# Optimization experiments

Measured on AMD Instinct MI355X. Metric: run time of the kernel, lower is better.

The kernel has to match this reference:

```python
import jax, jax.numpy as jnp
import numpy as np

B, N, C, H = 8, 1024, 1024, 16
D = C // H
DFF = 4 * C
EPS = 1e-6


def _ln(x):
    mu = jnp.mean(x, axis=-1, keepdims=True)
    var = jnp.mean(jnp.square(x - mu), axis=-1, keepdims=True)
    return (x - mu) / jnp.sqrt(var + EPS)


def _modulate(x, shift, scale):
    return x * (1 + scale) + shift


def setup_inputs() -> dict:
    key = jax.random.key(0)
    ks = jax.random.split(key, 12)
    s = 0.02
    inp = {
        "x": jax.random.normal(ks[0], (B, N, C), jnp.float32),
        "c": jax.random.normal(ks[1], (B, 1, C), jnp.float32),
        "causal_mask": jnp.tril(jnp.ones((N, N), jnp.int32))[None, None],  # [1,1,N,N]
        "qkv_w": jax.random.normal(ks[2], (3 * C, C), jnp.float32) * s,
        "qkv_b": jnp.zeros((3 * C,), jnp.float32),
        "proj_w": jax.random.normal(ks[3], (C, C), jnp.float32) * s,
        "proj_b": jnp.zeros((C,), jnp.float32),
        "fc1_w": jax.random.normal(ks[4], (DFF, C), jnp.float32) * s,
        "fc1_b": jnp.zeros((DFF,), jnp.float32),
        "fc2_w": jax.random.normal(ks[5], (C, DFF), jnp.float32) * s,
        "fc2_b": jnp.zeros((C,), jnp.float32),
        "ada_w": jax.random.normal(ks[6], (6 * C, C), jnp.float32) * s,
        "ada_b": jnp.zeros((6 * C,), jnp.float32),
    }
    return inp


def reference(x, c, causal_mask, qkv_w, qkv_b, proj_w, proj_b,
              fc1_w, fc1_b, fc2_w, fc2_b, ada_w, ada_b):
    # adaLN modulation: SiLU -> Linear(C -> 6C) -> chunk 6
    mod = jax.nn.silu(c) @ ada_w.T + ada_b  # [B,1,6C]
    (shift_msa, scale_msa, gate_msa,
     shift_mlp, scale_mlp, gate_mlp) = jnp.split(mod, 6, axis=-1)

    # --- causal attention ---
    y = _modulate(_ln(x), shift_msa, scale_msa)  # [B,N,C]
    qkv = y @ qkv_w.T + qkv_b                    # [B,N,3C]
    qkv = qkv.reshape(B, N, 3, H, D).transpose(2, 0, 3, 1, 4)  # [3,B,H,N,D]
    q, k, v = qkv[0], qkv[1], qkv[2]
    scale = D ** -0.5
    attn = jnp.einsum('bhnd,bhmd->bhnm', q, k) * scale  # [B,H,N,N]
    attn = jnp.where(causal_mask == 0, -jnp.inf, attn)
    attn = jax.nn.softmax(attn, axis=-1)
    o = jnp.einsum('bhnm,bhmd->bhnd', attn, v)
    o = o.transpose(0, 2, 1, 3).reshape(B, N, C)
    o = o @ proj_w.T + proj_b
    x = x + gate_msa * o

    # --- MLP ---
    z = _modulate(_ln(x), shift_mlp, scale_mlp)
    h = jax.nn.gelu(z @ fc1_w.T + fc1_b, approximate=True)
    m = h @ fc2_w.T + fc2_b
    x = x + gate_mlp * m
    return x
```

## Files before the change

kernel.cpp:

```cpp
#include <hip/hip_runtime.h>
#include <math.h>
#include <stdint.h>
#include <stddef.h>

namespace {

constexpr int kB = 8, kN = 1024, kC = 1024, kH = 16, kD = 64, kDFF = 4096;
constexpr int kM = kB * kN;
constexpr int k6C = 6 * kC;
constexpr float kQKScale = 0.18033688011112042f;
constexpr float kM8 = 8.0f;

typedef _Float16 half8 __attribute__((ext_vector_type(8)));
typedef _Float16 half4v __attribute__((ext_vector_type(4)));
typedef float f32x4 __attribute__((ext_vector_type(4)));
typedef int v4i __attribute__((ext_vector_type(4)));
typedef signed char i8;

__device__ inline void ld_lds16(const void* g, void* l) {
  __builtin_amdgcn_global_load_lds(
      (const __attribute__((address_space(1))) void*)g,
      (__attribute__((address_space(3))) void*)l, 16, 0, 0);
}

__device__ inline int xcd_swizzle(int flat, int nwg) {
  return (flat & 7) * (nwg >> 3) + (flat >> 3);
}

__device__ inline unsigned pack4_i8(float y0, float y1, float y2, float y3, float inv) {
  int q0 = (int)rintf(y0 * inv), q1 = (int)rintf(y1 * inv);
  int q2 = (int)rintf(y2 * inv), q3 = (int)rintf(y3 * inv);
  q0 = min(max(q0, -127), 127); q1 = min(max(q1, -127), 127);
  q2 = min(max(q2, -127), 127); q3 = min(max(q3, -127), 127);
  return (unsigned)(q0 & 0xFF) | ((unsigned)(q1 & 0xFF) << 8) |
         ((unsigned)(q2 & 0xFF) << 16) | ((unsigned)(q3 & 0xFF) << 24);
}

__global__ void cvt_f32_f16(const float* __restrict__ src, _Float16* __restrict__ dst) {
  size_t i = (size_t)blockIdx.x * 256 + threadIdx.x;
  float4 f = ((const float4*)src)[i];
  half4v h;
  h[0] = (_Float16)f.x; h[1] = (_Float16)f.y; h[2] = (_Float16)f.z; h[3] = (_Float16)f.w;
  ((half4v*)dst)[i] = h;
}

__global__ __launch_bounds__(256) void quant_w_kernel(
    const float* __restrict__ src, i8* __restrict__ dst, float* __restrict__ wscale) {
  int n = blockIdx.x, tid = threadIdx.x;
  const float* row = src + (size_t)n * kC;
  float4 f = ((const float4*)row)[tid];
  float m = fmaxf(fmaxf(fabsf(f.x), fabsf(f.y)), fmaxf(fabsf(f.z), fabsf(f.w)));
#pragma unroll
  for (int msk = 32; msk; msk >>= 1) m = fmaxf(m, __shfl_xor(m, msk));
  __shared__ float red[4];
  int w = tid >> 6, lane = tid & 63;
  if (lane == 0) red[w] = m;
  __syncthreads();
  m = fmaxf(fmaxf(red[0], red[1]), fmaxf(red[2], red[3]));
  m = fmaxf(m, 1e-12f);
  float inv = 127.f / m;
  ((unsigned*)(dst + (size_t)n * kC))[tid] = pack4_i8(f.x, f.y, f.z, f.w, inv);
  if (tid == 0) wscale[n] = m * (1.f / 127.f);
}

__global__ __launch_bounds__(256) void mod_kernel(
    const float* __restrict__ c, const float* __restrict__ ada_w,
    const float* __restrict__ ada_b, float* __restrict__ mod) {
  __shared__ float sc[kC];
  int b  = blockIdx.x / (k6C / 4);
  int j0 = (blockIdx.x % (k6C / 4)) * 4;
  int tid = threadIdx.x;
  for (int i = tid; i < kC; i += 256) {
    float v = c[b * kC + i];
    sc[i] = v / (1.f + expf(-v));
  }
  __syncthreads();
  int w = tid >> 6, lane = tid & 63;
  int j = j0 + w;
  const float* wr = ada_w + (size_t)j * kC;
  float acc = 0.f;
#pragma unroll
  for (int kk = 0; kk < kC / 64; ++kk) {
    int k = kk * 64 + lane;
    acc += sc[k] * wr[k];
  }
#pragma unroll
  for (int m = 32; m; m >>= 1) acc += __shfl_xor(acc, m);
  if (lane == 0) mod[b * k6C + j] = acc + ada_b[j];
}

template <typename T>
__global__ __launch_bounds__(256) void ln_mod_q_kernel(
    const T* __restrict__ x, const float* __restrict__ mod,
    i8* __restrict__ out, float* __restrict__ ascale,
    int shift_off, int scale_off) {
  int row = blockIdx.x;
  int b = row >> 10;
  const T* xr = x + (size_t)row * kC;
  int tid = threadIdx.x;
  int cc0 = tid * 4;
  float v[4];
  float s = 0.f, s2 = 0.f;
#pragma unroll
  for (int i = 0; i < 4; ++i) {
    v[i] = (float)xr[cc0 + i];
    s += v[i];
    s2 += v[i] * v[i];
  }
#pragma unroll
  for (int m = 32; m; m >>= 1) { s += __shfl_xor(s, m); s2 += __shfl_xor(s2, m); }
  __shared__ float red[8];
  __shared__ float redm[4];
  int w = tid >> 6, lane = tid & 63;
  if (lane == 0) { red[w] = s; red[4 + w] = s2; }
  __syncthreads();
  s  = red[0] + red[1] + red[2] + red[3];
  s2 = red[4] + red[5] + red[6] + red[7];
  float mu   = s * (1.f / kC);
  float var  = s2 * (1.f / kC) - mu * mu;
  float rstd = rsqrtf(var + 1e-6f);
  const float* mb = mod + (size_t)b * k6C;
  float y[4];
  float m = 0.f;
#pragma unroll
  for (int i = 0; i < 4; ++i) {
    y[i] = (v[i] - mu) * rstd * (1.f + mb[scale_off + cc0 + i]) + mb[shift_off + cc0 + i];
    m = fmaxf(m, fabsf(y[i]));
  }
#pragma unroll
  for (int msk = 32; msk; msk >>= 1) m = fmaxf(m, __shfl_xor(m, msk));
  if (lane == 0) redm[w] = m;
  __syncthreads();
  m = fmaxf(fmaxf(redm[0], redm[1]), fmaxf(redm[2], redm[3]));
  m = fmaxf(m, 1e-12f);
  float inv = 127.f / m;
  ((unsigned*)(out + (size_t)row * kC))[tid] = pack4_i8(y[0], y[1], y[2], y[3], inv);
  if (tid == 0) ascale[row] = m * (1.f / 127.f);
}

template <int EPI>
__global__ __launch_bounds__(256, 4) void gemm_i8_kernel(
    const i8* __restrict__ A, const i8* __restrict__ W,
    const float* __restrict__ ascale, const float* __restrict__ wscale,
    const float* __restrict__ bias, _Float16* __restrict__ outp,
    int M, int Nn, int K) {
  __shared__ __align__(16) i8 S[2 * 2 * 128 * 64];
  int tid = threadIdx.x;
  int nwg = (int)(gridDim.x * gridDim.y);
  int swz = xcd_swizzle((int)(blockIdx.y * gridDim.x + blockIdx.x), nwg);
  int bn = swz % (int)gridDim.x, bm = swz / (int)gridDim.x;
  int lane = tid & 63, w = tid >> 6;
  int l15 = lane & 15, quad = lane >> 4;
  int wr = (w >> 1) * 64, wc = (w & 1) * 64;

  v4i acc[4][4];
#pragma unroll
  for (int i = 0; i < 4; ++i)
#pragma unroll
    for (int j = 0; j < 4; ++j) acc[i][j] = (v4i){0, 0, 0, 0};

  const i8* Ag = A + (size_t)bm * 128 * K;
  const i8* Wg = W + (size_t)bn * 128 * K;
  int rg = lane >> 2;
  int gsl = lane & 3;

  int nk = K >> 6;
  {
    i8* As0 = S;
    i8* Bs0 = S + 128 * 64;
#pragma unroll
    for (int s = 0; s < 2; ++s) {
      int row = w * 32 + s * 16 + rg;
      int gc = (gsl ^ ((row >> 1) & 3)) * 16;
      ld_lds16(&Ag[(size_t)row * K + gc], &As0[(w * 32 + s * 16) * 64]);
      ld_lds16(&Wg[(size_t)row * K + gc], &Bs0[(w * 32 + s * 16) * 64]);
    }
  }
  __syncthreads();

  int cread = (quad ^ ((l15 >> 1) & 3)) * 16;
  for (int t = 0; t < nk; ++t) {
    const i8* As = S + (t & 1) * (2 * 128 * 64);
    const i8* Bs = As + 128 * 64;
    if (t + 1 < nk) {
      i8* Asn = S + ((t + 1) & 1) * (2 * 128 * 64);
      i8* Bsn = Asn + 128 * 64;
      int kt = (t + 1) << 6;
#pragma unroll
      for (int s = 0; s < 2; ++s) {
        int row = w * 32 + s * 16 + rg;
        int gc = (gsl ^ ((row >> 1) & 3)) * 16;
        ld_lds16(&Ag[(size_t)row * K + kt + gc], &Asn[(w * 32 + s * 16) * 64]);
        ld_lds16(&Wg[(size_t)row * K + kt + gc], &Bsn[(w * 32 + s * 16) * 64]);
      }
    }
    v4i af[4], bf[4];
#pragma unroll
    for (int i = 0; i < 4; ++i)
      af[i] = *(const v4i*)&As[(wr + i * 16 + l15) * 64 + cread];
#pragma unroll
    for (int j = 0; j < 4; ++j)
      bf[j] = *(const v4i*)&Bs[(wc + j * 16 + l15) * 64 + cread];
#pragma unroll
    for (int i = 0; i < 4; ++i)
#pragma unroll
      for (int j = 0; j < 4; ++j)
        acc[i][j] = __builtin_amdgcn_mfma_i32_16x16x64_i8(af[i], bf[j], acc[i][j], 0, 0, 0);
    __syncthreads();
  }

  _Float16* Cs = (_Float16*)S;
  int row0 = wr + quad * 4;
  int col0 = wc + l15;
#pragma unroll
  for (int i = 0; i < 4; ++i) {
#pragma unroll
    for (int j = 0; j < 4; ++j) {
      int colL = col0 + j * 16;
      int n = bn * 128 + colL;
      float ws = wscale[n];
      float bv = bias[n];
#pragma unroll
      for (int r = 0; r < 4; ++r) {
        int rowL = row0 + i * 16 + r;
        float as = ascale[bm * 128 + rowL];
        float v = (float)acc[i][j][r] * (as * ws) + bv;
        if constexpr (EPI == 0) {
          if (n < kC) v *= kQKScale;
        } else {
          float u = v + 0.044715f * v * v * v;
          float t = exp2f(-2.302208f * u);
          v = v * __builtin_amdgcn_rcpf(1.f + t);
        }
        Cs[rowL * 128 + (((colL >> 3) ^ (rowL & 7)) << 3) + (colL & 7)] = (_Float16)v;
      }
    }
  }
  __syncthreads();
#pragma unroll
  for (int p = 0; p < 8; ++p) {
    int r = (tid >> 4) + p * 16;
    int cc = tid & 15;
    half8 hv = *(const half8*)&Cs[r * 128 + ((cc ^ (r & 7)) << 3)];
    size_t gm = (size_t)(bm * 128 + r);
    int coff = bn * 128 + cc * 8;
    *(half8*)&outp[gm * Nn + coff] = hv;
  }
}

template <int EPI>
__global__ __launch_bounds__(256) void gemm_f16_kernel(
    const _Float16* __restrict__ A, const _Float16* __restrict__ W,
    const float* __restrict__ bias, void* __restrict__ outp,
    const void* __restrict__ resid, const float* __restrict__ mod,
    int M, int Nn, int K, int gate_off) {
  __shared__ __align__(16) _Float16 S[2 * 2 * 128 * 64];
  int tid = threadIdx.x;
  int nwg = (int)(gridDim.x * gridDim.y);
  int swz = xcd_swizzle((int)(blockIdx.y * gridDim.x + blockIdx.x), nwg);
  int bn = swz % (int)gridDim.x, bm = swz / (int)gridDim.x;
  int lane = tid & 63, w = tid >> 6;
  int l15 = lane & 15, quad = lane >> 4;
  int wr = (w >> 1) * 64, wc = (w & 1) * 64;

  f32x4 acc[4][4];
#pragma unroll
  for (int i = 0; i < 4; ++i)
#pragma unroll
    for (int j = 0; j < 4; ++j) acc[i][j] = (f32x4){0.f, 0.f, 0.f, 0.f};

  const _Float16* Ag = A + (size_t)bm * 128 * K;
  const _Float16* Wg = W + (size_t)bn * 128 * K;
  int r8 = lane >> 3;
  int jc = ((lane & 7) ^ r8) * 8;

  auto stage = [&](int buf, int kt) {
    _Float16* Asn = S + buf * (2 * 128 * 64);
    _Float16* Bsn = Asn + 128 * 64;
#pragma unroll
    for (int u = 0; u < 4; ++u) {
      int row = w * 32 + u * 8 + r8;
      ld_lds16(&Ag[(size_t)row * K + kt + jc], &Asn[(w * 32 + u * 8) * 64]);
      ld_lds16(&Wg[(size_t)row * K + kt + jc], &Bsn[(w * 32 + u * 8) * 64]);
    }
  };

  int nk = K / 64;
  stage(0, 0);
  stage(1, 64);

  for (int t = 0; t < nk; ++t) {
    if (t + 1 < nk) {
      asm volatile("s_waitcnt vmcnt(8)" ::: "memory");
    } else {
      asm volatile("s_waitcnt vmcnt(0)" ::: "memory");
    }
    __builtin_amdgcn_s_barrier();
    __builtin_amdgcn_sched_barrier(0);
    const _Float16* As = S + (t & 1) * (2 * 128 * 64);
    const _Float16* Bs = As + 128 * 64;
    half8 af[2][4], bf[2][4];
#pragma unroll
    for (int kk = 0; kk < 2; ++kk) {
#pragma unroll
      for (int i = 0; i < 4; ++i)
        af[kk][i] = *(const half8*)&As[(wr + i * 16 + l15) * 64 +
                                       (((kk * 4 + quad) ^ (l15 & 7)) * 8)];
#pragma unroll
      for (int j = 0; j < 4; ++j)
        bf[kk][j] = *(const half8*)&Bs[(wc + j * 16 + l15) * 64 +
                                       (((kk * 4 + quad) ^ (l15 & 7)) * 8)];
    }
    asm volatile("s_waitcnt lgkmcnt(0)" ::: "memory");
    __builtin_amdgcn_sched_barrier(0);
    __builtin_amdgcn_s_barrier();
    __builtin_amdgcn_sched_barrier(0);
    if (t + 2 < nk) stage(t & 1, (t + 2) * 64);
#pragma unroll
    for (int kk = 0; kk < 2; ++kk)
#pragma unroll
      for (int i = 0; i < 4; ++i)
#pragma unroll
        for (int j = 0; j < 4; ++j)
          acc[i][j] = __builtin_amdgcn_mfma_f32_16x16x32_f16(af[kk][i], bf[kk][j],
                                                             acc[i][j], 0, 0, 0);
  }

  _Float16* Cs = S;
  int row0 = wr + quad * 4;
  int col0 = wc + l15;
#pragma unroll
  for (int i = 0; i < 4; ++i) {
#pragma unroll
    for (int j = 0; j < 4; ++j) {
      int colL = col0 + j * 16;
      int n = bn * 128 + colL;
      float bv = bias[n];
#pragma unroll
      for (int r = 0; r < 4; ++r) {
        int rowL = row0 + i * 16 + r;
        float v = acc[i][j][r] + bv;
        Cs[rowL * 128 + (((colL >> 3) ^ (rowL & 7)) << 3) + (colL & 7)] = (_Float16)v;
      }
    }
  }
  __syncthreads();
  int b6 = (bm >> 3) * k6C + gate_off + bn * 128;
#pragma unroll
  for (int p = 0; p < 8; ++p) {
    int r = (tid >> 4) + p * 16;
    int cc = tid & 15;
    half8 hv = *(const half8*)&Cs[r * 128 + ((cc ^ (r & 7)) << 3)];
    size_t gm = (size_t)(bm * 128 + r);
    int coff = bn * 128 + cc * 8;
    if constexpr (EPI == 2) {
      const float* rp = &((const float*)resid)[gm * kC + coff];
      const float* gp = &mod[b6 + cc * 8];
      half8 ov;
#pragma unroll
      for (int e = 0; e < 8; ++e) ov[e] = (_Float16)(rp[e] + gp[e] * (float)hv[e]);
      *(half8*)&((_Float16*)outp)[gm * kC + coff] = ov;
    } else {
      const _Float16* rp = &((const _Float16*)resid)[gm * kC + coff];
      const float* gp = &mod[b6 + cc * 8];
      half8 rv = *(const half8*)rp;
      float ov[8];
#pragma unroll
      for (int e = 0; e < 8; ++e) ov[e] = (float)rv[e] + gp[e] * (float)hv[e];
      *(float4*)&((float*)outp)[gm * kC + coff] = *(float4*)&ov[0];
      *(float4*)&((float*)outp)[gm * kC + coff + 4] = *(float4*)&ov[4];
    }
  }
}

__global__ __launch_bounds__(256) void vtrans_kernel(
    const _Float16* __restrict__ qkv, _Float16* __restrict__ vT) {
  int nt = blockIdx.x, h = blockIdx.y, b = blockIdx.z;
  __shared__ _Float16 Ts[64 * 72];
  int tid = threadIdx.x;
  const _Float16* src = qkv + ((size_t)(b * kN + nt * 64)) * (3 * kC) + 2 * kC + h * 64;
#pragma unroll
  for (int u = 0; u < 2; ++u) {
    int idx = tid + u * 256;
    int r = idx >> 3, c8 = (idx & 7) * 8;
    *(uint4*)&Ts[r * 72 + c8] = *(const uint4*)&src[(size_t)r * (3 * kC) + c8];
  }
  __syncthreads();
  _Float16* dst = vT + (((size_t)(b * kH + h)) * 64) * kN + nt * 64;
#pragma unroll
  for (int u = 0; u < 2; ++u) {
    int idx = tid + u * 256;
    int d = idx >> 3, n8 = (idx & 7) * 8;
    half8 v;
#pragma unroll
    for (int e = 0; e < 8; ++e) v[e] = Ts[(n8 + e) * 72 + d];
    *(half8*)&dst[(size_t)d * kN + n8] = v;
  }
}

__global__ __launch_bounds__(256) void attn_kernel(
    const _Float16* __restrict__ qkv, const _Float16* __restrict__ vT,
    _Float16* __restrict__ o) {
  int nwg = (int)(gridDim.x * gridDim.y * gridDim.z);
  int flat = (int)((blockIdx.z * gridDim.y + blockIdx.y) * gridDim.x + blockIdx.x);
  int swz = xcd_swizzle(flat, nwg);
  int qt = swz % (int)gridDim.x;
  int tmp = swz / (int)gridDim.x;
  int h = tmp % (int)gridDim.y, b = tmp / (int)gridDim.y;
  __shared__ __align__(16) _Float16 Qs[128 * 64];
  __shared__ __align__(16) _Float16 Ks[64 * 64];
  __shared__ __align__(16) _Float16 Vs[64 * 64];
  __shared__ __align__(16) _Float16 Ps[128 * 72];
  int tid = threadIdx.x, lane = tid & 63, w = tid >> 6;
  int l15 = lane & 15, quad = lane >> 4;
  int wq = w * 32;
  int r8 = lane >> 3;
  int jc = ((lane & 7) ^ r8) * 8;

  const _Float16* Qg = qkv + ((size_t)(b * kN + qt * 128)) * (3 * kC) + h * kD;
  const _Float16* Kg = qkv + ((size_t)(b * kN)) * (3 * kC) + kC + h * kD;
  const _Float16* Vg = vT + ((size_t)(b * kH + h) * kD) * kN;

#pragma unroll
  for (int u = 0; u < 4; ++u)
    ld_lds16(&Qg[(size_t)(w * 32 + u * 8 + r8) * (3 * kC) + jc],
             &Qs[(w * 32 + u * 8) * 64]);
  __syncthreads();

  half8 aq[2][2];
#pragma unroll
  for (int i = 0; i < 2; ++i)
#pragma unroll
    for (int kk = 0; kk < 2; ++kk)
      aq[i][kk] = *(const half8*)&Qs[(wq + i * 16 + l15) * 64 +
                                     (((kk * 4 + quad) ^ (l15 & 7)) * 8)];

  f32x4 o_acc[2][4];
  f32x4 lsum[2];
#pragma unroll
  for (int i = 0; i < 2; ++i) {
    lsum[i] = (f32x4){0.f, 0.f, 0.f, 0.f};
#pragma unroll
    for (int dt = 0; dt < 4; ++dt) o_acc[i][dt] = (f32x4){0.f, 0.f, 0.f, 0.f};
  }
  half8 ones;
#pragma unroll
  for (int e = 0; e < 8; ++e) ones[e] = (_Float16)1.f;

  int jmax = 2 * qt + 2;
  for (int j = 0; j < jmax; ++j) {
#pragma unroll
    for (int u = 0; u < 2; ++u) {
      int row = w * 16 + u * 8 + r8;
      ld_lds16(&Kg[(size_t)(j * 64 + row) * (3 * kC) + jc], &Ks[(w * 16 + u * 8) * 64]);
      ld_lds16(&Vg[(size_t)row * kN + j * 64 + jc],         &Vs[(w * 16 + u * 8) * 64]);
    }
    __syncthreads();
    bool need_mask = (j >= 2 * qt);

    f32x4 s[2][4];
#pragma unroll
    for (int ct = 0; ct < 4; ++ct) {
      half8 b0 = *(const half8*)&Ks[(ct * 16 + l15) * 64 + ((quad ^ (l15 & 7)) * 8)];
      half8 b1 = *(const half8*)&Ks[(ct * 16 + l15) * 64 + (((4 + quad) ^ (l15 & 7)) * 8)];
#pragma unroll
      for (int i = 0; i < 2; ++i) {
        f32x4 t = (f32x4){0.f, 0.f, 0.f, 0.f};
        t = __builtin_amdgcn_mfma_f32_16x16x32_f16(aq[i][0], b0, t, 0, 0, 0);
        t = __builtin_amdgcn_mfma_f32_16x16x32_f16(aq[i][1], b1, t, 0, 0, 0);
        s[i][ct] = t;
      }
    }

#pragma unroll
    for (int i = 0; i < 2; ++i)
#pragma unroll
      for (int ct = 0; ct < 4; ++ct)
#pragma unroll
        for (int r = 0; r < 4; ++r) {
          float p = exp2f(fminf(s[i][ct][r] - kM8, 14.f));
          if (need_mask) {
            int kg = j * 64 + ct * 16 + l15;
            int qg = qt * 128 + wq + i * 16 + quad * 4 + r;
            if (kg > qg) p = 0.f;
          }
          Ps[(wq + i * 16 + quad * 4 + r) * 72 + ct * 16 + l15] = (_Float16)p;
        }

    half8 ap[2][2];
#pragma unroll
    for (int i = 0; i < 2; ++i) {
      ap[i][0] = *(const half8*)&Ps[(wq + i * 16 + l15) * 72 + quad * 8];
      ap[i][1] = *(const half8*)&Ps[(wq + i * 16 + l15) * 72 + 32 + quad * 8];
      lsum[i] = __builtin_amdgcn_mfma_f32_16x16x32_f16(ap[i][0], ones, lsum[i], 0, 0, 0);
      lsum[i] = __builtin_amdgcn_mfma_f32_16x16x32_f16(ap[i][1], ones, lsum[i], 0, 0, 0);
    }
#pragma unroll
    for (int dt = 0; dt < 4; ++dt) {
      half8 bv0 = *(const half8*)&Vs[(dt * 16 + l15) * 64 + ((quad ^ (l15 & 7)) * 8)];
      half8 bv1 = *(const half8*)&Vs[(dt * 16 + l15) * 64 + (((4 + quad) ^ (l15 & 7)) * 8)];
#pragma unroll
      for (int i = 0; i < 2; ++i) {
        o_acc[i][dt] = __builtin_amdgcn_mfma_f32_16x16x32_f16(ap[i][0], bv0, o_acc[i][dt], 0, 0, 0);
        o_acc[i][dt] = __builtin_amdgcn_mfma_f32_16x16x32_f16(ap[i][1], bv1, o_acc[i][dt], 0, 0, 0);
      }
    }
    __syncthreads();
  }

#pragma unroll
  for (int i = 0; i < 2; ++i) {
    float rl[4];
#pragma unroll
    for (int r = 0; r < 4; ++r) rl[r] = __builtin_amdgcn_rcpf(lsum[i][r]);
#pragma unroll
    for (int dt = 0; dt < 4; ++dt)
#pragma unroll
      for (int r = 0; r < 4; ++r) {
        int q = qt * 128 + wq + i * 16 + quad * 4 + r;
        o[((size_t)(b * kN + q)) * kC + h * kD + dt * 16 + l15] =
            (_Float16)(o_acc[i][dt][r] * rl[r]);
      }
  }
}

}

extern "C" void kernel_launch(void* const* d_in, const int* in_sizes, int n_in,
                              void* d_out, int out_size, void* d_ws, size_t ws_size,
                              hipStream_t stream) {
  const float* x      = (const float*)d_in[0];
  const float* c      = (const float*)d_in[1];
  const float* qkv_w  = (const float*)d_in[3];
  const float* qkv_b  = (const float*)d_in[4];
  const float* proj_w = (const float*)d_in[5];
  const float* proj_b = (const float*)d_in[6];
  const float* fc1_w  = (const float*)d_in[7];
  const float* fc1_b  = (const float*)d_in[8];
  const float* fc2_w  = (const float*)d_in[9];
  const float* fc2_b  = (const float*)d_in[10];
  const float* ada_w  = (const float*)d_in[11];
  const float* ada_b  = (const float*)d_in[12];
  float* out = (float*)d_out;

  char* ws = (char*)d_ws;
  float*    mod     = (float*)(ws);
  i8*       w_qkv   = (i8*)(ws + 196608);
  i8*       w_fc1   = (i8*)(ws + 3342336);
  _Float16* w_proj  = (_Float16*)(ws + 7536640);
  _Float16* w_fc2   = (_Float16*)(ws + 9633792);
  i8*       bufA    = (i8*)(ws + 18022400);
  float*    ascale  = (float*)(ws + 26411008);
  float*    ws_qkv  = (float*)(ws + 26443776);
  float*    ws_fc1  = (float*)(ws + 26456064);
  _Float16* vT      = (_Float16*)(ws + 26509312);
  _Float16* x2h     = (_Float16*)(ws + 26509312);
  _Float16* bufO    = (_Float16*)(ws + 43286528);
  _Float16* qkvh    = (_Float16*)(ws + 60063744);
  _Float16* hbuf    = (_Float16*)(ws + 60063744);

  quant_w_kernel<<<3 * kC, 256, 0, stream>>>(qkv_w, w_qkv, ws_qkv);
  quant_w_kernel<<<kDFF, 256, 0, stream>>>(fc1_w, w_fc1, ws_fc1);
  cvt_f32_f16<<<kC * kC / 1024, 256, 0, stream>>>(proj_w, w_proj);
  cvt_f32_f16<<<kC * kDFF / 1024, 256, 0, stream>>>(fc2_w, w_fc2);
  mod_kernel<<<kB * (k6C / 4), 256, 0, stream>>>(c, ada_w, ada_b, mod);
  ln_mod_q_kernel<float><<<kM, 256, 0, stream>>>(x, mod, bufA, ascale, 0, kC);
  gemm_i8_kernel<0><<<dim3(3 * kC / 128, kM / 128), 256, 0, stream>>>(
      bufA, w_qkv, ascale, ws_qkv, qkv_b, qkvh, kM, 3 * kC, kC);
  vtrans_kernel<<<dim3(kN / 64, kH, kB), 256, 0, stream>>>(qkvh, vT);
  attn_kernel<<<dim3(kN / 128, kH, kB), 256, 0, stream>>>(qkvh, vT, bufO);
  gemm_f16_kernel<2><<<dim3(kC / 128, kM / 128), 256, 0, stream>>>(
      bufO, w_proj, proj_b, x2h, x, mod, kM, kC, kC, 2 * kC);
  ln_mod_q_kernel<_Float16><<<kM, 256, 0, stream>>>(x2h, mod, bufA, ascale, 3 * kC, 4 * kC);
  gemm_i8_kernel<1><<<dim3(kDFF / 128, kM / 128), 256, 0, stream>>>(
      bufA, w_fc1, ascale, ws_fc1, fc1_b, hbuf, kM, kDFF, kC);
  gemm_f16_kernel<3><<<dim3(kC / 128, kM / 128), 256, 0, stream>>>(
      hbuf, w_fc2, fc2_b, out, x2h, mod, kM, kC, kDFF, 5 * kC);
}
```

Measured before the change: 467.3 us.

## Deepen prefetch pipelines in int8 GEMM and attention with vmcnt-based waits

The int8 GEMM main loop now issues its global-to-LDS loads two K-tiles ahead instead of one. It waits with explicit vmcnt counters and uses a single barrier per step, placed after the fragment reads, before reissuing loads into the freed buffer. The attention kernel double-buffers its K/V tiles in one merged shared array and prefetches tile j+2 once the current V fragments are in registers. It also raises launch bounds to three blocks per CU. The aim is to hide global load latency behind MFMA work, at the cost of hand-tuned waitcnt logic that could race if the counts are wrong, plus more LDS and register pressure.

```diff
diff --git a/kernel.cpp b/kernel.cpp
--- a/kernel.cpp
+++ b/kernel.cpp
@@ -164,36 +164,33 @@
   int rg = lane >> 2;
   int gsl = lane & 3;
 
-  int nk = K >> 6;
-  {
-    i8* As0 = S;
-    i8* Bs0 = S + 128 * 64;
+  auto stage = [&](int buf, int kt) {
+    i8* As = S + buf * (2 * 128 * 64);
+    i8* Bs = As + 128 * 64;
 #pragma unroll
     for (int s = 0; s < 2; ++s) {
       int row = w * 32 + s * 16 + rg;
       int gc = (gsl ^ ((row >> 1) & 3)) * 16;
-      ld_lds16(&Ag[(size_t)row * K + gc], &As0[(w * 32 + s * 16) * 64]);
-      ld_lds16(&Wg[(size_t)row * K + gc], &Bs0[(w * 32 + s * 16) * 64]);
-    }
-  }
-  __syncthreads();
+      ld_lds16(&Ag[(size_t)row * K + kt + gc], &As[(w * 32 + s * 16) * 64]);
+      ld_lds16(&Wg[(size_t)row * K + kt + gc], &Bs[(w * 32 + s * 16) * 64]);
+    }
+  };
+
+  int nk = K >> 6;
+  stage(0, 0);
+  stage(1, 64);
 
   int cread = (quad ^ ((l15 >> 1) & 3)) * 16;
   for (int t = 0; t < nk; ++t) {
+    if (t + 1 < nk) {
+      asm volatile("s_waitcnt vmcnt(4)" ::: "memory");
+    } else {
+      asm volatile("s_waitcnt vmcnt(0)" ::: "memory");
+    }
+    __builtin_amdgcn_s_barrier();
+    __builtin_amdgcn_sched_barrier(0);
     const i8* As = S + (t & 1) * (2 * 128 * 64);
     const i8* Bs = As + 128 * 64;
-    if (t + 1 < nk) {
-      i8* Asn = S + ((t + 1) & 1) * (2 * 128 * 64);
-      i8* Bsn = Asn + 128 * 64;
-      int kt = (t + 1) << 6;
-#pragma unroll
-      for (int s = 0; s < 2; ++s) {
-        int row = w * 32 + s * 16 + rg;
-        int gc = (gsl ^ ((row >> 1) & 3)) * 16;
-        ld_lds16(&Ag[(size_t)row * K + kt + gc], &Asn[(w * 32 + s * 16) * 64]);
-        ld_lds16(&Wg[(size_t)row * K + kt + gc], &Bsn[(w * 32 + s * 16) * 64]);
-      }
-    }
     v4i af[4], bf[4];
 #pragma unroll
     for (int i = 0; i < 4; ++i)
@@ -201,12 +198,16 @@
 #pragma unroll
     for (int j = 0; j < 4; ++j)
       bf[j] = *(const v4i*)&Bs[(wc + j * 16 + l15) * 64 + cread];
+    asm volatile("s_waitcnt lgkmcnt(0)" ::: "memory");
+    __builtin_amdgcn_sched_barrier(0);
+    __builtin_amdgcn_s_barrier();
+    __builtin_amdgcn_sched_barrier(0);
+    if (t + 2 < nk) stage(t & 1, (t + 2) << 6);
 #pragma unroll
     for (int i = 0; i < 4; ++i)
 #pragma unroll
       for (int j = 0; j < 4; ++j)
         acc[i][j] = __builtin_amdgcn_mfma_i32_16x16x64_i8(af[i], bf[j], acc[i][j], 0, 0, 0);
-    __syncthreads();
   }
 
   _Float16* Cs = (_Float16*)S;
@@ -398,7 +399,7 @@
   }
 }
 
-__global__ __launch_bounds__(256) void attn_kernel(
+__global__ __launch_bounds__(256, 3) void attn_kernel(
     const _Float16* __restrict__ qkv, const _Float16* __restrict__ vT,
     _Float16* __restrict__ o) {
   int nwg = (int)(gridDim.x * gridDim.y * gridDim.z);
@@ -407,10 +408,8 @@
   int qt = swz % (int)gridDim.x;
   int tmp = swz / (int)gridDim.x;
   int h = tmp % (int)gridDim.y, b = tmp / (int)gridDim.y;
-  __shared__ __align__(16) _Float16 Qs[128 * 64];
-  __shared__ __align__(16) _Float16 Ks[64 * 64];
-  __shared__ __align__(16) _Float16 Vs[64 * 64];
-  __shared__ __align__(16) _Float16 Ps[128 * 72];
+  __shared__ __align__(16) _Float16 S[2 * 8192 + 128 * 72];
+  _Float16* Ps = S + 16384;
   int tid = threadIdx.x, lane = tid & 63, w = tid >> 6;
   int l15 = lane & 15, quad = lane >> 4;
   int wq = w * 32;
@@ -421,19 +420,34 @@
   const _Float16* Kg = qkv + ((size_t)(b * kN)) * (3 * kC) + kC + h * kD;
   const _Float16* Vg = vT + ((size_t)(b * kH + h) * kD) * kN;
 
+  auto stage_kv = [&](_Float16* dstK, int j) {
+#pragma unroll
+    for (int u = 0; u < 2; ++u) {
+      int row = w * 16 + u * 8 + r8;
+      ld_lds16(&Kg[(size_t)(j * 64 + row) * (3 * kC) + jc], &dstK[(w * 16 + u * 8) * 64]);
+      ld_lds16(&Vg[(size_t)row * kN + j * 64 + jc], &dstK[4096 + (w * 16 + u * 8) * 64]);
+    }
+  };
+
 #pragma unroll
   for (int u = 0; u < 4; ++u)
     ld_lds16(&Qg[(size_t)(w * 32 + u * 8 + r8) * (3 * kC) + jc],
-             &Qs[(w * 32 + u * 8) * 64]);
-  __syncthreads();
+             &S[(w * 32 + u * 8) * 64]);
+  stage_kv(S + 8192, 0);
+  asm volatile("s_waitcnt vmcnt(4)" ::: "memory");
+  __builtin_amdgcn_s_barrier();
 
   half8 aq[2][2];
 #pragma unroll
   for (int i = 0; i < 2; ++i)
 #pragma unroll
     for (int kk = 0; kk < 2; ++kk)
-      aq[i][kk] = *(const half8*)&Qs[(wq + i * 16 + l15) * 64 +
-                                     (((kk * 4 + quad) ^ (l15 & 7)) * 8)];
+      aq[i][kk] = *(const half8*)&S[(wq + i * 16 + l15) * 64 +
+                                    (((kk * 4 + quad) ^ (l15 & 7)) * 8)];
+  asm volatile("s_waitcnt lgkmcnt(0)" ::: "memory");
+  __builtin_amdgcn_sched_barrier(0);
+  __builtin_amdgcn_s_barrier();
+  stage_kv(S, 1);
 
   f32x4 o_acc[2][4];
   f32x4 lsum[2];
@@ -449,13 +463,15 @@
 
   int jmax = 2 * qt + 2;
   for (int j = 0; j < jmax; ++j) {
-#pragma unroll
-    for (int u = 0; u < 2; ++u) {
-      int row = w * 16 + u * 8 + r8;
-      ld_lds16(&Kg[(size_t)(j * 64 + row) * (3 * kC) + jc], &Ks[(w * 16 + u * 8) * 64]);
-      ld_lds16(&Vg[(size_t)row * kN + j * 64 + jc],         &Vs[(w * 16 + u * 8) * 64]);
-    }
-    __syncthreads();
+    if (j + 1 < jmax) {
+      asm volatile("s_waitcnt vmcnt(4)" ::: "memory");
+    } else {
+      asm volatile("s_waitcnt vmcnt(0)" ::: "memory");
+    }
+    __builtin_amdgcn_s_barrier();
+    __builtin_amdgcn_sched_barrier(0);
+    const _Float16* Ks = (j & 1) ? S : S + 8192;
+    const _Float16* Vs = Ks + 4096;
     bool need_mask = (j >= 2 * qt);
 
     f32x4 s[2][4];
@@ -487,6 +503,19 @@
           Ps[(wq + i * 16 + quad * 4 + r) * 72 + ct * 16 + l15] = (_Float16)p;
         }
 
+    half8 bv0[4], bv1[4];
+#pragma unroll
+    for (int dt = 0; dt < 4; ++dt) {
+      bv0[dt] = *(const half8*)&Vs[(dt * 16 + l15) * 64 + ((quad ^ (l15 & 7)) * 8)];
+      bv1[dt] = *(const half8*)&Vs[(dt * 16 + l15) * 64 + (((4 + quad) ^ (l15 & 7)) * 8)];
+    }
+    asm volatile("s_waitcnt lgkmcnt(0)" ::: "memory");
+    __builtin_amdgcn_sched_barrier(0);
+    __builtin_amdgcn_s_barrier();
+    __builtin_amdgcn_sched_barrier(0);
+    if (j + 2 < jmax)
+      stage_kv((j & 1) ? S : S + 8192, j + 2);
+
     half8 ap[2][2];
 #pragma unroll
     for (int i = 0; i < 2; ++i) {
@@ -496,16 +525,12 @@
       lsum[i] = __builtin_amdgcn_mfma_f32_16x16x32_f16(ap[i][1], ones, lsum[i], 0, 0, 0);
     }
 #pragma unroll
-    for (int dt = 0; dt < 4; ++dt) {
-      half8 bv0 = *(const half8*)&Vs[(dt * 16 + l15) * 64 + ((quad ^ (l15 & 7)) * 8)];
-      half8 bv1 = *(const half8*)&Vs[(dt * 16 + l15) * 64 + (((4 + quad) ^ (l15 & 7)) * 8)];
+    for (int dt = 0; dt < 4; ++dt)
 #pragma unroll
       for (int i = 0; i < 2; ++i) {
-        o_acc[i][dt] = __builtin_amdgcn_mfma_f32_16x16x32_f16(ap[i][0], bv0, o_acc[i][dt], 0, 0, 0);
-        o_acc[i][dt] = __builtin_amdgcn_mfma_f32_16x16x32_f16(ap[i][1], bv1, o_acc[i][dt], 0, 0, 0);
+        o_acc[i][dt] = __builtin_amdgcn_mfma_f32_16x16x32_f16(ap[i][0], bv0[dt], o_acc[i][dt], 0, 0, 0);
+        o_acc[i][dt] = __builtin_amdgcn_mfma_f32_16x16x32_f16(ap[i][1], bv1[dt], o_acc[i][dt], 0, 0, 0);
       }
-    }
-    __syncthreads();
   }
 
 #pragma unroll
```

New measurement: 456.9 us. 2.2% less time.
